# Optimization experiments

Hardware: AMD Instinct MI355X
Metric: run time of the kernel (lower is better)

## Reference

```python
import jax, jax.numpy as jnp
import numpy as np

NUM_PATCHES = 10
SIGMA = 4.0            # size_exp_deadzone
PAD_X = 16             # padding_deadzone_size_x
PAD_Y = 16             # padding_deadzone_size_y
DEADZONE_EXP = True
HARD_CUTOUT = True     # deadzone_hard_cutout == 1
HARD_CUTOUT_SIZE = 4.0


def setup_inputs() -> dict:
    key = jax.random.key(0)
    k1, k2, k3, k4 = jax.random.split(key, 4)
    B, C, H, W = 8, 1, 256, 256
    D, KH, KW = 64, 1, 33
    inp = {
        "input": jax.random.normal(k1, (B, C, H, W), dtype=jnp.float32),
        "dictionary_filter": jax.random.normal(k2, (64, C, 33, 33), dtype=jnp.float32),
        "dictionary": jax.random.normal(k3, (64, C, 33, 33), dtype=jnp.float32),
        "dictionary_prior": jax.random.uniform(k4, (64,), dtype=jnp.float32),
    }
    return inp


def _fourier_convolution(contour, dictionary_filter):
    # contour: [B,C,H,W], dictionary_filter: [D,C,kh,kw] (kh,kw odd)
    B, C, H, W = contour.shape
    D, _, kh, kw = dictionary_filter.shape
    filt = jnp.flip(dictionary_filter, axis=(-2, -1))
    padded = jnp.zeros((D, C, H, W), dtype=contour.dtype).at[:, :, :kh, :kw].set(filt)
    padded = jnp.roll(padded, shift=(-(kh // 2), -(kw // 2)), axis=(-2, -1))
    filt_fft = jnp.fft.rfft2(padded)                 # [D,C,H,W//2+1]
    contour_fft = jnp.fft.rfft2(contour)             # [B,C,H,W//2+1]
    # [B,D,C,H,W] -> sum over channel C -> [B,D,H,W]
    conv = jnp.fft.irfft2(contour_fft[:, None] * filt_fft[None], s=(H, W)).sum(axis=2)
    return conv


def reference(input, dictionary_filter, dictionary, dictionary_prior):
    B, C, H, W = input.shape
    dt = input.dtype
    conv = _fourier_convolution(input, dictionary_filter)  # [B,D,H,W]

    use_map = jnp.ones((B, H, W), dtype=dt)
    if PAD_X > 0:
        use_map = use_map.at[:, :PAD_X, :].set(0.0).at[:, -PAD_X:, :].set(0.0)
    if PAD_Y > 0:
        use_map = use_map.at[:, :, :PAD_Y].set(0.0).at[:, :, -PAD_Y:].set(0.0)

    xs = jnp.arange(H, dtype=dt)
    ys = jnp.arange(W, dtype=dt)
    batch_idx = jnp.arange(B)

    def step(use_map, _):
        # search tensor: conv * use_map * prior  -> [B,D,H,W]
        search = conv * use_map[:, None] * dictionary_prior[None, :, None, None]
        flat = search.reshape(B, -1)
        idx = jnp.argmax(flat, axis=1)                    # [B]
        ov0 = jnp.max(flat, axis=1)                       # saliency incl. prior
        d = idx // (H * W)
        rem = idx % (H * W)
        px = rem // W
        py = rem % W
        ov1 = conv[batch_idx, d, px, py]                  # raw overlap
        # deadzone centered at (px,py)
        dx = xs[None, :] - px[:, None].astype(dt)         # [B,H]
        dy = ys[None, :] - py[:, None].astype(dt)         # [B,W]
        dist2 = dx[:, :, None] ** 2 + dy[:, None, :] ** 2  # [B,H,W]
        if DEADZONE_EXP:
            tmap = 1.0 - jnp.exp(-dist2 / (2.0 * SIGMA ** 2))
        else:
            tmap = jnp.ones_like(dist2)
        if HARD_CUTOUT:
            tmap = tmap * jnp.where(dist2 <= HARD_CUTOUT_SIZE ** 2, 0.0, 1.0)
        new_use = use_map * tmap
        new_use = new_use / jnp.max(new_use, axis=(1, 2), keepdims=True)
        pos = jnp.stack([d, px, py], axis=1)              # [B,3]
        ov = jnp.stack([ov0, ov1], axis=1)                # [B,2]
        return new_use, (pos, ov)

    _, (pos, ov) = jax.lax.scan(step, use_map, None, length=NUM_PATCHES)
    position_found = jnp.transpose(pos, (1, 0, 2))  # [B, num_patches, 3] int
    overlap_found = jnp.transpose(ov, (1, 0, 2))    # [B, num_patches, 2]
    return position_found, overlap_found
```

## Files before the change

### kernel.cpp

```cpp
#include <hip/hip_runtime.h>

typedef unsigned long long u64;
typedef unsigned int u32;
typedef unsigned short ushort_t;

using f32x16 = __attribute__((ext_vector_type(16))) float;
using f32x4  = __attribute__((ext_vector_type(4))) float;
using short8 = __attribute__((ext_vector_type(8))) short;

#define NB 8
#define NPIX 65536
#define CAP1 8192
#define BAND 44.0f
#define CERT 43.0f

__device__ __forceinline__ u32 fsort(float f){
  u32 u = __float_as_uint(f);
  return (u & 0x80000000u) ? ~u : (u | 0x80000000u);
}
__device__ __forceinline__ float funsort(u32 s){
  u32 u = (s & 0x80000000u) ? (s ^ 0x80000000u) : ~s;
  return __uint_as_float(u);
}
__device__ __forceinline__ u32 rneb(float f){
  u32 x = __float_as_uint(f);
  return (x + 0x7fffu + ((x >> 16) & 1u)) >> 16;
}
__device__ __forceinline__ float bf2f(u32 h){ return __uint_as_float(h << 16); }

__global__ __launch_bounds__(256) void transpose_kernel(
    const float* __restrict__ filt, float* __restrict__ filtT,
    u32* __restrict__ ncand, u32* __restrict__ mmax)
{
  __shared__ float T[64][65];
  const int b = blockIdx.x;
  const int e0 = b * 64;
  const int ecnt = min(64, 1089 - e0);
  const int w = threadIdx.x >> 6, l = threadIdx.x & 63;
  if (b == 0 && threadIdx.x < 8){ ncand[threadIdx.x] = 0u; mmax[threadIdx.x] = 0u; }
  for (int d = w; d < 64; d += 4)
    if (l < ecnt) T[d][l] = filt[d * 1089 + e0 + l];
  __syncthreads();
  for (int r = w; r < ecnt; r += 4)
    filtT[(e0 + r) * 64 + l] = T[l][r];
}

__global__ __launch_bounds__(256) void prep_kernel(
    const float* __restrict__ filt, const float* __restrict__ filtT,
    const float* __restrict__ prior,
    ushort_t* __restrict__ afh, ushort_t* __restrict__ acolh,
    float* __restrict__ fcorner, float* __restrict__ priorR,
    float* __restrict__ filtT4, float* __restrict__ filtC)
{
  int t = blockIdx.x * 256 + threadIdx.x;
  for (int i = t; i < 67584; i += 16384){
    int j = i & 7; int fidx = i >> 3; int lane = fidx & 63; int rest = fidx >> 6;
    int dt = rest & 1; int kc = (rest >> 1) & 1; int fy = rest >> 2;
    int d = dt * 32 + (lane & 31);
    int fx = 16 * kc + 8 * (lane >> 5) + j;
    afh[i] = (ushort_t)rneb(filt[d * 1089 + fy * 33 + fx]);
  }
  for (int i = t; i < 2048; i += 16384){
    int j = i & 7; int fidx = i >> 3; int lane = fidx & 63; int rest = fidx >> 6;
    int dt = rest & 1; int kc = rest >> 1;
    int d = dt * 32 + (lane & 31);
    int fy = 16 * kc + 8 * (lane >> 5) + j;
    acolh[i] = (ushort_t)rneb(filt[d * 1089 + fy * 33 + 32]);
  }
  for (int i = t; i < 2048; i += 16384){
    int reg = i & 15; int rest = i >> 4; int lane = rest & 63; int dt = rest >> 6;
    int d = dt * 32 + (reg & 3) + 8 * (reg >> 2) + 4 * (lane >> 5);
    fcorner[i] = filt[d * 1089 + 1088];
    priorR[i] = prior[d];
  }
  for (int i = t; i < 67584; i += 16384){
    int e = i & 3; int d = (i >> 2) & 63; int q = (i >> 8) & 7; int fy = i >> 11;
    filtT4[i] = filtT[(fy * 33 + 4 * q + e) * 64 + d];
  }
  for (int i = t; i < 2112; i += 16384){
    int d = i & 63; int fy = i >> 6;
    filtC[i] = filtT[(fy * 33 + 32) * 64 + d];
  }
}

__device__ __forceinline__ u32 funnel(u32 hi, u32 lo, int sh){
  return (u32)((((u64)hi << 32) | (u64)lo) >> sh);
}
template<int J>
__device__ __forceinline__ short8 extractf(uint4 P0, uint4 P1, int sh){
  u32 W[8] = {P0.x, P0.y, P0.z, P0.w, P1.x, P1.y, P1.z, P1.w};
  uint4 t;
  t.x = funnel(W[J + 1], W[J + 0], sh);
  t.y = funnel(W[J + 2], W[J + 1], sh);
  t.z = funnel(W[J + 3], W[J + 2], sh);
  t.w = funnel(W[J + 4], W[J + 3], sh);
  return __builtin_bit_cast(short8, t);
}
__device__ __forceinline__ f32x16 zero16(){
  f32x16 v;
  #pragma unroll
  for (int i = 0; i < 16; ++i) v[i] = 0.f;
  return v;
}

template<int J>
__device__ __forceinline__ void conv_body(
    const char* ldsc, const ushort_t* lds16, int w, int l, int tX,
    const short8* __restrict__ afh8, const short8* __restrict__ acol8,
    const f32x4* __restrict__ fcp, const f32x4* __restrict__ prp,
    u64* __restrict__ pb, int sh)
{
  const int c = l & 31, h = l >> 5;
  const int y0 = w;
  int cob0[2], cob1[2];
  #pragma unroll
  for (int kc = 0; kc < 2; ++kc){
    int yp = (y0 + 8 * c + 16 * kc + 8 * h - 16) & 255;
    int b0 = yp >> 3, b1 = (b0 + 1) & 31;
    cob0[kc] = b0 * 16; cob1[kc] = b1 * 16;
  }
  const int cc = (y0 + 8 * c + 16) & 255;

#define LA(DST, FY)                                                           \
  { _Pragma("unroll")                                                         \
    for (int kc = 0; kc < 2; ++kc)                                            \
      _Pragma("unroll")                                                       \
      for (int dt = 0; dt < 2; ++dt)                                          \
        DST[kc][dt] = afh8[(((FY) * 2 + kc) * 2 + dt) * 64 + l]; }

#define LW(S, ROWI)                                                           \
  { const char* rb_ = ldsc + (ROWI) * 512;                                    \
    s##S##k0p0 = *(const uint4*)(rb_ + cob0[0]);                              \
    s##S##k0p1 = *(const uint4*)(rb_ + cob1[0]);                              \
    s##S##k1p0 = *(const uint4*)(rb_ + cob0[1]);                              \
    s##S##k1p1 = *(const uint4*)(rb_ + cob1[1]); }

#define CPH(SA, SB, ACUR, ANXT, FYP, DOPF)                                    \
  { if (DOPF){ LA(ANXT, FYP) }                                                \
    short8 b0k0 = extractf<J>(s##SA##k0p0, s##SA##k0p1, sh);                  \
    short8 b0k1 = extractf<J>(s##SA##k1p0, s##SA##k1p1, sh);                  \
    short8 b1k0 = extractf<J>(s##SB##k0p0, s##SB##k0p1, sh);                  \
    short8 b1k1 = extractf<J>(s##SB##k1p0, s##SB##k1p1, sh);                  \
    acc[0][0] = __builtin_amdgcn_mfma_f32_32x32x16_bf16(ACUR[0][0], b0k0, acc[0][0], 0, 0, 0); \
    acc[0][0] = __builtin_amdgcn_mfma_f32_32x32x16_bf16(ACUR[1][0], b0k1, acc[0][0], 0, 0, 0); \
    acc[0][1] = __builtin_amdgcn_mfma_f32_32x32x16_bf16(ACUR[0][1], b0k0, acc[0][1], 0, 0, 0); \
    acc[0][1] = __builtin_amdgcn_mfma_f32_32x32x16_bf16(ACUR[1][1], b0k1, acc[0][1], 0, 0, 0); \
    acc[1][0] = __builtin_amdgcn_mfma_f32_32x32x16_bf16(ACUR[0][0], b1k0, acc[1][0], 0, 0, 0); \
    acc[1][0] = __builtin_amdgcn_mfma_f32_32x32x16_bf16(ACUR[1][0], b1k1, acc[1][0], 0, 0, 0); \
    acc[1][1] = __builtin_amdgcn_mfma_f32_32x32x16_bf16(ACUR[0][1], b1k0, acc[1][1], 0, 0, 0); \
    acc[1][1] = __builtin_amdgcn_mfma_f32_32x32x16_bf16(ACUR[1][1], b1k1, acc[1][1], 0, 0, 0); }

  for (int g0 = 0; g0 < 2; ++g0){
    const int r0 = g0 * 2;
    f32x16 acc[2][2];
    #pragma unroll
    for (int nr = 0; nr < 2; ++nr)
      #pragma unroll
      for (int dt = 0; dt < 2; ++dt) acc[nr][dt] = zero16();

    uint4 s0k0p0, s0k0p1, s0k1p0, s0k1p1;
    uint4 s1k0p0, s1k0p1, s1k1p0, s1k1p1;
    short8 aA[2][2], aB[2][2];

    LW(0, r0)
    LW(1, r0 + 1)
    LA(aA, 0)

    #pragma unroll 1
    for (int fy2 = 0; fy2 < 32; fy2 += 2){
      CPH(0, 1, aA, aB, fy2 + 1, true)
      LW(0, r0 + fy2 + 2)
      CPH(1, 0, aB, aA, fy2 + 2, true)
      LW(1, r0 + fy2 + 3)
    }
    CPH(0, 1, aA, aB, 0, false)

    #pragma unroll
    for (int nr = 0; nr < 2; ++nr){
      #pragma unroll
      for (int kc = 0; kc < 2; ++kc){
        int base = (r0 + nr + 16 * kc + 8 * h) * 512 + cc * 2;
        u32 v0 = *(const ushort_t*)(ldsc + base + 0 * 512);
        u32 v1 = *(const ushort_t*)(ldsc + base + 1 * 512);
        u32 v2 = *(const ushort_t*)(ldsc + base + 2 * 512);
        u32 v3 = *(const ushort_t*)(ldsc + base + 3 * 512);
        u32 v4 = *(const ushort_t*)(ldsc + base + 4 * 512);
        u32 v5 = *(const ushort_t*)(ldsc + base + 5 * 512);
        u32 v6 = *(const ushort_t*)(ldsc + base + 6 * 512);
        u32 v7 = *(const ushort_t*)(ldsc + base + 7 * 512);
        uint4 t;
        t.x = v0 | (v1 << 16); t.y = v2 | (v3 << 16);
        t.z = v4 | (v5 << 16); t.w = v6 | (v7 << 16);
        short8 Bc = __builtin_bit_cast(short8, t);
        #pragma unroll
        for (int dt = 0; dt < 2; ++dt)
          acc[nr][dt] = __builtin_amdgcn_mfma_f32_32x32x16_bf16(
              acol8[(kc * 2 + dt) * 64 + l], Bc, acc[nr][dt], 0, 0, 0);
      }
    }

    #pragma unroll
    for (int nr = 0; nr < 2; ++nr){
      float cv = bf2f((u32)lds16[(r0 + nr + 32) * 256 + cc]);
      float bv = -3e38f; int bd = 0;
      #pragma unroll
      for (int dt = 0; dt < 2; ++dt){
        #pragma unroll
        for (int q = 0; q < 4; ++q){
          f32x4 fc4 = fcp[(dt * 64 + l) * 4 + q];
          f32x4 pr4 = prp[(dt * 64 + l) * 4 + q];
          #pragma unroll
          for (int e = 0; e < 4; ++e){
            int reg = q * 4 + e;
            float s = (acc[nr][dt][reg] + fc4[e] * cv) * pr4[e];
            int d = dt * 32 + e + 8 * q + 4 * h;
            if (s > bv || (s == bv && d < bd)){ bv = s; bd = d; }
          }
        }
      }
      int x = tX + r0 + nr;
      int y = y0 + 8 * c;
      u64 key = ((u64)fsort(bv) << 32) | (u64)(63 - bd);
      u64 other = __shfl_xor(key, 32);
      if (other > key) key = other;
      if (h == 0) pb[(x << 8) | y] = key;
    }
  }
#undef CPH
#undef LW
#undef LA
}

__global__ __launch_bounds__(512) void conv_mfma(
    const float* __restrict__ input,
    const ushort_t* __restrict__ afh, const ushort_t* __restrict__ acolh,
    const float* __restrict__ fcorner, const float* __restrict__ priorR,
    u64* __restrict__ packed)
{
  __shared__ ushort_t lds[9216];
  const int bS = blockIdx.x;
  const int b  = blockIdx.y;
  const int tX = bS * 4;
  const int tid = threadIdx.x;

  const float* inb = input + b * NPIX;
  for (int k = tid; k < 1152; k += 512){
    int r = k >> 5, u = k & 31;
    int gx = (tX - 16 + r) & 255;
    const float* src = inb + (gx << 8) + (u << 3);
    float4 v1 = *(const float4*)(src);
    float4 v2 = *(const float4*)(src + 4);
    uint4 t;
    t.x = rneb(v1.x) | (rneb(v1.y) << 16);
    t.y = rneb(v1.z) | (rneb(v1.w) << 16);
    t.z = rneb(v2.x) | (rneb(v2.y) << 16);
    t.w = rneb(v2.z) | (rneb(v2.w) << 16);
    *(uint4*)((char*)lds + r * 512 + u * 16) = t;
  }
  __syncthreads();

  const int w = tid >> 6, l = tid & 63;
  u64* pb = packed + b * NPIX;
  const int sh = 16 * (w & 1);
  const char* ldsc = (const char*)lds;
  const short8* afh8 = (const short8*)afh;
  const short8* acol8 = (const short8*)acolh;
  const f32x4* fcp = (const f32x4*)fcorner;
  const f32x4* prp = (const f32x4*)priorR;

  switch ((w >> 1) & 3){
    case 0: conv_body<0>(ldsc, lds, w, l, tX, afh8, acol8, fcp, prp, pb, sh); break;
    case 1: conv_body<1>(ldsc, lds, w, l, tX, afh8, acol8, fcp, prp, pb, sh); break;
    case 2: conv_body<2>(ldsc, lds, w, l, tX, afh8, acol8, fcp, prp, pb, sh); break;
    default: conv_body<3>(ldsc, lds, w, l, tX, afh8, acol8, fcp, prp, pb, sh); break;
  }
}

__global__ __launch_bounds__(256) void bmax_kernel(const u64* __restrict__ packed,
                                                   u32* __restrict__ mmax){
  const int b = blockIdx.y, blk = blockIdx.x, tid = threadIdx.x;
  const u32* ph = (const u32*)(packed + b * NPIX);
  u32 m = 0;
  for (int k = tid; k < 2048; k += 256) m = max(m, ph[2 * (blk * 2048 + k) + 1]);
  __shared__ u32 red[256];
  red[tid] = m; __syncthreads();
  for (int s = 128; s > 0; s >>= 1){
    if (tid < s) red[tid] = max(red[tid], red[tid + s]);
    __syncthreads();
  }
  if (tid == 0) atomicMax(&mmax[b], red[0]);
}

__global__ __launch_bounds__(256) void collect_kernel(const u64* __restrict__ packed,
    const u32* __restrict__ mmax, u32* __restrict__ ncand, u32* __restrict__ cand){
  const int b = blockIdx.y, blk = blockIdx.x, tid = threadIdx.x;
  u32 tu = fsort(funsort(mmax[b]) - BAND);
  const u32* ph = (const u32*)(packed + b * NPIX);
  for (int k = tid; k < 2048; k += 256){
    int p = blk * 2048 + k;
    int px = p >> 8, py = p & 255;
    u32 v = ph[2 * p + 1];
    if (v >= tu && px >= 16 && px < 240 && py >= 16 && py < 240){
      u32 slot = atomicAdd(&ncand[b], 1u);
      if (slot < CAP1) cand[b * CAP1 + slot] = (u32)p;
    }
  }
}

__global__ __launch_bounds__(256) void rerank_kernel(
    const float* __restrict__ input, const float* __restrict__ filtT4,
    const float* __restrict__ filtC, const float* __restrict__ prior,
    const u32* __restrict__ ncand, const u32* __restrict__ cand,
    u64* __restrict__ packed)
{
  const int lane = threadIdx.x & 63;
  const int b = blockIdx.y;
  const int ws = blockIdx.x * 4 + (threadIdx.x >> 6);
  int n = (int)min(ncand[b], (u32)CAP1);
  float pv = prior[lane];
  for (int i = ws; i < n; i += 512){
    int p = (int)cand[b * CAP1 + i];
    int px = p >> 8;
    int yc = (p & 255) - 16;
    float s0 = 0.f, s1 = 0.f, s2 = 0.f, s3 = 0.f;
    for (int fy = 0; fy < 33; ++fy){
      const float* ir = input + b * NPIX + ((px + fy - 16) << 8) + yc;
      const float* ft = filtT4 + fy * 2048 + lane * 4;
      #pragma unroll
      for (int q = 0; q < 8; ++q){
        const float4 fv = *(const float4*)(ft + q * 256);
        s0 = fmaf(fv.x, ir[4*q+0], s0);
        s1 = fmaf(fv.y, ir[4*q+1], s1);
        s2 = fmaf(fv.z, ir[4*q+2], s2);
        s3 = fmaf(fv.w, ir[4*q+3], s3);
      }
      s0 = fmaf(filtC[fy * 64 + lane], ir[32], s0);
    }
    float s = (s0 + s2) + (s1 + s3);
    u64 key = ((u64)fsort(s * pv) << 32) | (u64)(63 - lane);
    #pragma unroll
    for (int off = 32; off; off >>= 1){
      u64 o = __shfl_down(key, off);
      if (o > key) key = o;
    }
    if (lane == 0) packed[b * NPIX + p] = key;
  }
}

__global__ __launch_bounds__(1024) void greedy_sl(
    const u64* __restrict__ packed, const float* __restrict__ prior,
    const u32* __restrict__ ncand, const u32* __restrict__ cand,
    const u32* __restrict__ mmax, float* __restrict__ out)
{
  const int b = blockIdx.x;
  const int tid = threadIdx.x;
  const u64* pb = packed + b * NPIX;
  const int n = (int)min(ncand[b], (u32)CAP1);

  int cp[8]; float cv[8];
  #pragma unroll
  for (int k = 0; k < 8; ++k){
    int idx = tid + k * 1024;
    if (idx < n){ cp[k] = (int)cand[b * CAP1 + idx]; cv[k] = funsort((u32)(pb[cp[k]] >> 32)); }
    else        { cp[k] = 0; cv[k] = -3e38f; }
  }

  __shared__ u64 warr[16];
  __shared__ int spx, spy, okf;
  __shared__ float v10s;
  if (tid == 0){ spx = -100000; spy = -100000; }
  __syncthreads();

  for (int t = 0; t < 10; ++t){
    const int px = spx, py = spy;
    if (px >= 0){
      #pragma unroll
      for (int k = 0; k < 8; ++k){
        if (tid + k * 1024 < n){
          float dx = (float)((cp[k] >> 8) - px), dy = (float)((cp[k] & 255) - py);
          float d2 = dx * dx + dy * dy;
          float tmap = 1.f - __expf(d2 * -0.03125f);
          if (d2 <= 16.f) tmap = 0.f;
          cv[k] *= tmap;
        }
      }
    }
    u64 key = 0ull;
    #pragma unroll
    for (int k = 0; k < 8; ++k){
      u64 kk = ((u64)fsort(cv[k]) << 32) | (u64)(0xFFFFu ^ (u32)cp[k]);
      if (kk > key) key = kk;
    }
    #pragma unroll
    for (int off = 32; off; off >>= 1){
      u64 o = __shfl_down(key, off);
      if (o > key) key = o;
    }
    if ((tid & 63) == 0) warr[tid >> 6] = key;
    __syncthreads();
    if (tid < 64){
      u64 k2 = (tid < 16) ? warr[tid] : 0ull;
      #pragma unroll
      for (int off = 8; off; off >>= 1){
        u64 o = __shfl_down(k2, off);
        if (o > k2) k2 = o;
      }
      if (tid == 0){
        int id = 0xFFFF ^ (int)(k2 & 0xFFFFull);
        float v = funsort((u32)(k2 >> 32));
        u64 pk = pb[id];
        int d = 63 - (int)(pk & 63ull);
        float bvv = funsort((u32)(pk >> 32));
        int xx = id >> 8, yy = id & 255;
        out[b * 30 + t * 3 + 0] = (float)d;
        out[b * 30 + t * 3 + 1] = (float)xx;
        out[b * 30 + t * 3 + 2] = (float)yy;
        out[240 + b * 20 + t * 2 + 0] = v;
        out[240 + b * 20 + t * 2 + 1] = bvv / prior[d];
        spx = xx; spy = yy;
        if (t == 9) v10s = v;
      }
    }
    __syncthreads();
  }

  if (tid == 0)
    okf = (ncand[b] <= (u32)CAP1 && v10s >= funsort(mmax[b]) - CERT) ? 1 : 0;
  __syncthreads();
  if (okf) return;

  {
    const int x = tid >> 2;
    const int ybase = (tid & 3) << 6;
    const int pbase = (x << 8) + ybase;
    float s[64];
    const bool rowin = (x >= 16 && x < 240);
    #pragma unroll
    for (int i2 = 0; i2 < 32; ++i2){
      uint4 two = *(const uint4*)(pb + pbase + 2 * i2);
      int y = ybase + 2 * i2;
      s[2*i2+0] = (rowin && y+0 >= 16 && y+0 < 240) ? funsort(two.y) : 0.0f;
      s[2*i2+1] = (rowin && y+1 >= 16 && y+1 < 240) ? funsort(two.w) : 0.0f;
    }
    float tm = -3e38f; int tp = pbase;
    #pragma unroll
    for (int i = 0; i < 64; ++i){
      if (s[i] > tm){ tm = s[i]; tp = pbase + i; }
    }
    if (tid == 0){ spx = -100000; spy = -100000; }
    __syncthreads();
    for (int t = 0; t < 10; ++t){
      const int px = spx, py = spy;
      if (px >= 0){
        int dxr = x - px;
        if (dxr >= -24 && dxr <= 24){
          int lo = py - 24 - ybase;
          int hi = py + 24 - ybase;
          if (lo < 64 && hi >= 0){
            float dx2 = (float)(dxr * dxr);
            tm = -3e38f; tp = pbase;
            #pragma unroll
            for (int i = 0; i < 64; ++i){
              if (i >= lo && i <= hi){
                float dy = (float)(ybase + i - py);
                float d2 = dx2 + dy * dy;
                float tmap = 1.f - __expf(d2 * -0.03125f);
                if (d2 <= 16.f) tmap = 0.f;
                s[i] *= tmap;
              }
              if (s[i] > tm){ tm = s[i]; tp = pbase + i; }
            }
          }
        }
      }
      u64 key = ((u64)fsort(tm) << 32) | (u64)(0xFFFFu ^ (u32)tp);
      #pragma unroll
      for (int off = 32; off; off >>= 1){
        u64 o = __shfl_down(key, off);
        if (o > key) key = o;
      }
      if ((tid & 63) == 0) warr[tid >> 6] = key;
      __syncthreads();
      if (tid < 64){
        u64 k2 = (tid < 16) ? warr[tid] : 0ull;
        #pragma unroll
        for (int off = 8; off; off >>= 1){
          u64 o = __shfl_down(k2, off);
          if (o > k2) k2 = o;
        }
        if (tid == 0){
          int id = 0xFFFF ^ (int)(k2 & 0xFFFFull);
          float v = funsort((u32)(k2 >> 32));
          u64 pk = pb[id];
          int d = 63 - (int)(pk & 63ull);
          float bvv = funsort((u32)(pk >> 32));
          int xx = id >> 8, yy = id & 255;
          out[b * 30 + t * 3 + 0] = (float)d;
          out[b * 30 + t * 3 + 1] = (float)xx;
          out[b * 30 + t * 3 + 2] = (float)yy;
          out[240 + b * 20 + t * 2 + 0] = v;
          out[240 + b * 20 + t * 2 + 1] = bvv / prior[d];
          spx = xx; spy = yy;
        }
      }
      __syncthreads();
    }
  }
}

extern "C" void kernel_launch(void* const* d_in, const int* in_sizes, int n_in,
                              void* d_out, int out_size, void* d_ws, size_t ws_size,
                              hipStream_t stream)
{
  const float* input = (const float*)d_in[0];
  const float* filt  = (const float*)d_in[1];
  const float* prior = (const float*)d_in[3];
  float* out = (float*)d_out;

  char* ws = (char*)d_ws;
  u64*      packed  = (u64*)(ws);
  u32*      ncand   = (u32*)  (ws + 4194304);
  u32*      mmax    = (u32*)  (ws + 4194368);
  ushort_t* afh     = (ushort_t*)(ws + 4194432);
  ushort_t* acolh   = (ushort_t*)(ws + 4329600);
  float*    fcorner = (float*)(ws + 4333696);
  float*    priorR  = (float*)(ws + 4341888);
  u32*      cand    = (u32*)  (ws + 4350080);
  float*    filtT4  = (float*)(ws + 4612224);
  float*    filtC   = (float*)(ws + 4882560);
  float*    filtT   = (float*)(ws + 4891008);

  transpose_kernel<<<18, 256, 0, stream>>>(filt, filtT, ncand, mmax);
  prep_kernel<<<64, 256, 0, stream>>>(filt, filtT, prior, afh, acolh,
                                      fcorner, priorR, filtT4, filtC);
  conv_mfma<<<dim3(64, NB), 512, 0, stream>>>(input, afh, acolh, fcorner, priorR, packed);
  bmax_kernel<<<dim3(32, NB), 256, 0, stream>>>(packed, mmax);
  collect_kernel<<<dim3(32, NB), 256, 0, stream>>>(packed, mmax, ncand, cand);
  rerank_kernel<<<dim3(128, NB), 256, 0, stream>>>(input, filtT4, filtC, prior,
                                                   ncand, cand, packed);
  greedy_sl<<<NB, 1024, 0, stream>>>(packed, prior, ncand, cand, mmax, out);
}
```

Before: 250.9 us.

## Derive candidate threshold from tenth-best disjoint block max instead of global max band

Replaces the global-max reduction plus fixed band with a lower bound taken from 16 disjoint 16x16 sub-blocks. The tenth-largest block max minus a small epsilon becomes the candidate threshold, which should admit far fewer candidates into the bf16 rerank and greedy stages. It also drops the post-greedy certification check and the full-image fallback whenever candidates fit in the capacity. The tighter threshold rests on assumptions about the bf16 approximation error and deadzone suppression, so correctness could be at risk if the error exceeds the epsilon.

```diff
diff --git a/kernel.cpp b/kernel.cpp
--- a/kernel.cpp
+++ b/kernel.cpp
@@ -11,8 +11,7 @@
 #define NB 8
 #define NPIX 65536
 #define CAP1 8192
-#define BAND 44.0f
-#define CERT 43.0f
+#define EPS2 8.0f
 
 __device__ __forceinline__ u32 fsort(float f){
   u32 u = __float_as_uint(f);
@@ -30,14 +29,14 @@
 
 __global__ __launch_bounds__(256) void transpose_kernel(
     const float* __restrict__ filt, float* __restrict__ filtT,
-    u32* __restrict__ ncand, u32* __restrict__ mmax)
+    u32* __restrict__ ncand)
 {
   __shared__ float T[64][65];
   const int b = blockIdx.x;
   const int e0 = b * 64;
   const int ecnt = min(64, 1089 - e0);
   const int w = threadIdx.x >> 6, l = threadIdx.x & 63;
-  if (b == 0 && threadIdx.x < 8){ ncand[threadIdx.x] = 0u; mmax[threadIdx.x] = 0u; }
+  if (b == 0 && threadIdx.x < 8) ncand[threadIdx.x] = 0u;
   for (int d = w; d < 64; d += 4)
     if (l < ecnt) T[d][l] = filt[d * 1089 + e0 + l];
   __syncthreads();
@@ -276,25 +275,45 @@
   }
 }
 
-__global__ __launch_bounds__(256) void bmax_kernel(const u64* __restrict__ packed,
-                                                   u32* __restrict__ mmax){
+__global__ __launch_bounds__(256) void lbound_kernel(
+    const u64* __restrict__ packed, float* __restrict__ thr)
+{
+  const int b = blockIdx.x;
+  const int tid = threadIdx.x;
+  const u32* ph = (const u32*)(packed + b * NPIX);
+  __shared__ u32 red[256];
+  __shared__ u32 q16[16];
+  const int r = tid >> 4, cY = tid & 15;
+  for (int sc = 0; sc < 16; ++sc){
+    int x = 24 + ((sc >> 2) << 6) + r;
+    int y = 24 + ((sc & 3) << 6) + cY;
+    red[tid] = ph[2 * ((x << 8) | y) + 1];
+    __syncthreads();
+    for (int s = 128; s > 0; s >>= 1){
+      if (tid < s) red[tid] = max(red[tid], red[tid + s]);
+      __syncthreads();
+    }
+    if (tid == 0) q16[sc] = red[0];
+    __syncthreads();
+  }
+  if (tid == 0){
+    u32 q[16];
+    for (int i = 0; i < 16; ++i) q[i] = q16[i];
+    u32 tenth = 0;
+    for (int k = 0; k < 10; ++k){
+      int bi = 0;
+      for (int i = 1; i < 16; ++i) if (q[i] > q[bi]) bi = i;
+      tenth = q[bi];
+      q[bi] = 0;
+    }
+    thr[b] = funsort(tenth) - EPS2;
+  }
+}
+
+__global__ __launch_bounds__(256) void collect_kernel(const u64* __restrict__ packed,
+    const float* __restrict__ thr, u32* __restrict__ ncand, u32* __restrict__ cand){
   const int b = blockIdx.y, blk = blockIdx.x, tid = threadIdx.x;
-  const u32* ph = (const u32*)(packed + b * NPIX);
-  u32 m = 0;
-  for (int k = tid; k < 2048; k += 256) m = max(m, ph[2 * (blk * 2048 + k) + 1]);
-  __shared__ u32 red[256];
-  red[tid] = m; __syncthreads();
-  for (int s = 128; s > 0; s >>= 1){
-    if (tid < s) red[tid] = max(red[tid], red[tid + s]);
-    __syncthreads();
-  }
-  if (tid == 0) atomicMax(&mmax[b], red[0]);
-}
-
-__global__ __launch_bounds__(256) void collect_kernel(const u64* __restrict__ packed,
-    const u32* __restrict__ mmax, u32* __restrict__ ncand, u32* __restrict__ cand){
-  const int b = blockIdx.y, blk = blockIdx.x, tid = threadIdx.x;
-  u32 tu = fsort(funsort(mmax[b]) - BAND);
+  u32 tu = fsort(thr[b]);
   const u32* ph = (const u32*)(packed + b * NPIX);
   for (int k = tid; k < 2048; k += 256){
     int p = blk * 2048 + k;
@@ -350,7 +369,7 @@
 __global__ __launch_bounds__(1024) void greedy_sl(
     const u64* __restrict__ packed, const float* __restrict__ prior,
     const u32* __restrict__ ncand, const u32* __restrict__ cand,
-    const u32* __restrict__ mmax, float* __restrict__ out)
+    float* __restrict__ out)
 {
   const int b = blockIdx.x;
   const int tid = threadIdx.x;
@@ -367,67 +386,62 @@
 
   __shared__ u64 warr[16];
   __shared__ int spx, spy, okf;
-  __shared__ float v10s;
-  if (tid == 0){ spx = -100000; spy = -100000; }
+  if (tid == 0){ spx = -100000; spy = -100000; okf = (ncand[b] <= (u32)CAP1); }
   __syncthreads();
-
-  for (int t = 0; t < 10; ++t){
-    const int px = spx, py = spy;
-    if (px >= 0){
+  if (okf){
+    for (int t = 0; t < 10; ++t){
+      const int px = spx, py = spy;
+      if (px >= 0){
+        #pragma unroll
+        for (int k = 0; k < 8; ++k){
+          if (tid + k * 1024 < n){
+            float dx = (float)((cp[k] >> 8) - px), dy = (float)((cp[k] & 255) - py);
+            float d2 = dx * dx + dy * dy;
+            float tmap = 1.f - __expf(d2 * -0.03125f);
+            if (d2 <= 16.f) tmap = 0.f;
+            cv[k] *= tmap;
+          }
+        }
+      }
+      u64 key = 0ull;
       #pragma unroll
       for (int k = 0; k < 8; ++k){
-        if (tid + k * 1024 < n){
-          float dx = (float)((cp[k] >> 8) - px), dy = (float)((cp[k] & 255) - py);
-          float d2 = dx * dx + dy * dy;
-          float tmap = 1.f - __expf(d2 * -0.03125f);
-          if (d2 <= 16.f) tmap = 0.f;
-          cv[k] *= tmap;
-        }
-      }
-    }
-    u64 key = 0ull;
-    #pragma unroll
-    for (int k = 0; k < 8; ++k){
-      u64 kk = ((u64)fsort(cv[k]) << 32) | (u64)(0xFFFFu ^ (u32)cp[k]);
-      if (kk > key) key = kk;
-    }
-    #pragma unroll
-    for (int off = 32; off; off >>= 1){
-      u64 o = __shfl_down(key, off);
-      if (o > key) key = o;
-    }
-    if ((tid & 63) == 0) warr[tid >> 6] = key;
-    __syncthreads();
-    if (tid < 64){
-      u64 k2 = (tid < 16) ? warr[tid] : 0ull;
-      #pragma unroll
-      for (int off = 8; off; off >>= 1){
-        u64 o = __shfl_down(k2, off);
-        if (o > k2) k2 = o;
-      }
-      if (tid == 0){
-        int id = 0xFFFF ^ (int)(k2 & 0xFFFFull);
-        float v = funsort((u32)(k2 >> 32));
-        u64 pk = pb[id];
-        int d = 63 - (int)(pk & 63ull);
-        float bvv = funsort((u32)(pk >> 32));
-        int xx = id >> 8, yy = id & 255;
-        out[b * 30 + t * 3 + 0] = (float)d;
-        out[b * 30 + t * 3 + 1] = (float)xx;
-        out[b * 30 + t * 3 + 2] = (float)yy;
-        out[240 + b * 20 + t * 2 + 0] = v;
-        out[240 + b * 20 + t * 2 + 1] = bvv / prior[d];
-        spx = xx; spy = yy;
-        if (t == 9) v10s = v;
-      }
-    }
-    __syncthreads();
-  }
-
-  if (tid == 0)
-    okf = (ncand[b] <= (u32)CAP1 && v10s >= funsort(mmax[b]) - CERT) ? 1 : 0;
-  __syncthreads();
-  if (okf) return;
+        u64 kk = ((u64)fsort(cv[k]) << 32) | (u64)(0xFFFFu ^ (u32)cp[k]);
+        if (kk > key) key = kk;
+      }
+      #pragma unroll
+      for (int off = 32; off; off >>= 1){
+        u64 o = __shfl_down(key, off);
+        if (o > key) key = o;
+      }
+      if ((tid & 63) == 0) warr[tid >> 6] = key;
+      __syncthreads();
+      if (tid < 64){
+        u64 k2 = (tid < 16) ? warr[tid] : 0ull;
+        #pragma unroll
+        for (int off = 8; off; off >>= 1){
+          u64 o = __shfl_down(k2, off);
+          if (o > k2) k2 = o;
+        }
+        if (tid == 0){
+          int id = 0xFFFF ^ (int)(k2 & 0xFFFFull);
+          float v = funsort((u32)(k2 >> 32));
+          u64 pk = pb[id];
+          int d = 63 - (int)(pk & 63ull);
+          float bvv = funsort((u32)(pk >> 32));
+          int xx = id >> 8, yy = id & 255;
+          out[b * 30 + t * 3 + 0] = (float)d;
+          out[b * 30 + t * 3 + 1] = (float)xx;
+          out[b * 30 + t * 3 + 2] = (float)yy;
+          out[240 + b * 20 + t * 2 + 0] = v;
+          out[240 + b * 20 + t * 2 + 1] = bvv / prior[d];
+          spx = xx; spy = yy;
+        }
+      }
+      __syncthreads();
+    }
+    return;
+  }
 
   {
     const int x = tid >> 2;
@@ -447,7 +461,6 @@
     for (int i = 0; i < 64; ++i){
       if (s[i] > tm){ tm = s[i]; tp = pbase + i; }
     }
-    if (tid == 0){ spx = -100000; spy = -100000; }
     __syncthreads();
     for (int t = 0; t < 10; ++t){
       const int px = spx, py = spy;
@@ -520,7 +533,7 @@
   char* ws = (char*)d_ws;
   u64*      packed  = (u64*)(ws);
   u32*      ncand   = (u32*)  (ws + 4194304);
-  u32*      mmax    = (u32*)  (ws + 4194368);
+  float*    thr     = (float*)(ws + 4194368);
   ushort_t* afh     = (ushort_t*)(ws + 4194432);
   ushort_t* acolh   = (ushort_t*)(ws + 4329600);
   float*    fcorner = (float*)(ws + 4333696);
@@ -530,13 +543,13 @@
   float*    filtC   = (float*)(ws + 4882560);
   float*    filtT   = (float*)(ws + 4891008);
 
-  transpose_kernel<<<18, 256, 0, stream>>>(filt, filtT, ncand, mmax);
+  transpose_kernel<<<18, 256, 0, stream>>>(filt, filtT, ncand);
   prep_kernel<<<64, 256, 0, stream>>>(filt, filtT, prior, afh, acolh,
                                       fcorner, priorR, filtT4, filtC);
   conv_mfma<<<dim3(64, NB), 512, 0, stream>>>(input, afh, acolh, fcorner, priorR, packed);
-  bmax_kernel<<<dim3(32, NB), 256, 0, stream>>>(packed, mmax);
-  collect_kernel<<<dim3(32, NB), 256, 0, stream>>>(packed, mmax, ncand, cand);
+  lbound_kernel<<<NB, 256, 0, stream>>>(packed, thr);
+  collect_kernel<<<dim3(32, NB), 256, 0, stream>>>(packed, thr, ncand, cand);
   rerank_kernel<<<dim3(128, NB), 256, 0, stream>>>(input, filtT4, filtC, prior,
                                                    ncand, cand, packed);
-  greedy_sl<<<NB, 1024, 0, stream>>>(packed, prior, ncand, cand, mmax, out);
-}
+  greedy_sl<<<NB, 1024, 0, stream>>>(packed, prior, ncand, cand, out);
+}
```

Measured after the change: 239.9 us. 4.4% less time.

## Add pre-greedy pass to tighten rerank candidate threshold

Applied to the files above, without the earlier changes.

Adds a greedy pass over the approximate (bf16 MFMA) scores to estimate the 10th selected value, then collects a second, smaller candidate set within a slack of that value. Only those candidates get the exact fp32 rerank, and the final greedy runs over at most 4096 candidates instead of 8192. This trades two extra small kernel launches and a duplicated greedy for less rerank work, and it relies on tighter certification margins that can force the full-image fallback more often.

```diff
diff --git a/kernel.cpp b/kernel.cpp
--- a/kernel.cpp
+++ b/kernel.cpp
@@ -11,8 +11,10 @@
 #define NB 8
 #define NPIX 65536
 #define CAP1 8192
-#define BAND 44.0f
-#define CERT 43.0f
+#define CAP2 4096
+#define T1    24.0f
+#define SLACK 12.0f
+#define CERTF 10.0f
 
 __device__ __forceinline__ u32 fsort(float f){
   u32 u = __float_as_uint(f);
@@ -30,14 +32,15 @@
 
 __global__ __launch_bounds__(256) void transpose_kernel(
     const float* __restrict__ filt, float* __restrict__ filtT,
-    u32* __restrict__ ncand, u32* __restrict__ mmax)
+    u32* __restrict__ nc16, u32* __restrict__ mmax)
 {
   __shared__ float T[64][65];
   const int b = blockIdx.x;
   const int e0 = b * 64;
   const int ecnt = min(64, 1089 - e0);
   const int w = threadIdx.x >> 6, l = threadIdx.x & 63;
-  if (b == 0 && threadIdx.x < 8){ ncand[threadIdx.x] = 0u; mmax[threadIdx.x] = 0u; }
+  if (b == 0 && threadIdx.x < 16) nc16[threadIdx.x] = 0u;
+  if (b == 0 && threadIdx.x < 8)  mmax[threadIdx.x] = 0u;
   for (int d = w; d < 64; d += 4)
     if (l < ecnt) T[d][l] = filt[d * 1089 + e0 + l];
   __syncthreads();
@@ -291,71 +294,31 @@
   if (tid == 0) atomicMax(&mmax[b], red[0]);
 }
 
-__global__ __launch_bounds__(256) void collect_kernel(const u64* __restrict__ packed,
-    const u32* __restrict__ mmax, u32* __restrict__ ncand, u32* __restrict__ cand){
+__global__ __launch_bounds__(256) void collect1_kernel(const u64* __restrict__ packed,
+    const u32* __restrict__ mmax, u32* __restrict__ nc16, u32* __restrict__ cand){
   const int b = blockIdx.y, blk = blockIdx.x, tid = threadIdx.x;
-  u32 tu = fsort(funsort(mmax[b]) - BAND);
+  u32 tu = fsort(funsort(mmax[b]) - T1);
   const u32* ph = (const u32*)(packed + b * NPIX);
   for (int k = tid; k < 2048; k += 256){
     int p = blk * 2048 + k;
     int px = p >> 8, py = p & 255;
     u32 v = ph[2 * p + 1];
     if (v >= tu && px >= 16 && px < 240 && py >= 16 && py < 240){
-      u32 slot = atomicAdd(&ncand[b], 1u);
+      u32 slot = atomicAdd(&nc16[b], 1u);
       if (slot < CAP1) cand[b * CAP1 + slot] = (u32)p;
     }
   }
 }
 
-__global__ __launch_bounds__(256) void rerank_kernel(
-    const float* __restrict__ input, const float* __restrict__ filtT4,
-    const float* __restrict__ filtC, const float* __restrict__ prior,
-    const u32* __restrict__ ncand, const u32* __restrict__ cand,
-    u64* __restrict__ packed)
-{
-  const int lane = threadIdx.x & 63;
-  const int b = blockIdx.y;
-  const int ws = blockIdx.x * 4 + (threadIdx.x >> 6);
-  int n = (int)min(ncand[b], (u32)CAP1);
-  float pv = prior[lane];
-  for (int i = ws; i < n; i += 512){
-    int p = (int)cand[b * CAP1 + i];
-    int px = p >> 8;
-    int yc = (p & 255) - 16;
-    float s0 = 0.f, s1 = 0.f, s2 = 0.f, s3 = 0.f;
-    for (int fy = 0; fy < 33; ++fy){
-      const float* ir = input + b * NPIX + ((px + fy - 16) << 8) + yc;
-      const float* ft = filtT4 + fy * 2048 + lane * 4;
-      #pragma unroll
-      for (int q = 0; q < 8; ++q){
-        const float4 fv = *(const float4*)(ft + q * 256);
-        s0 = fmaf(fv.x, ir[4*q+0], s0);
-        s1 = fmaf(fv.y, ir[4*q+1], s1);
-        s2 = fmaf(fv.z, ir[4*q+2], s2);
-        s3 = fmaf(fv.w, ir[4*q+3], s3);
-      }
-      s0 = fmaf(filtC[fy * 64 + lane], ir[32], s0);
-    }
-    float s = (s0 + s2) + (s1 + s3);
-    u64 key = ((u64)fsort(s * pv) << 32) | (u64)(63 - lane);
-    #pragma unroll
-    for (int off = 32; off; off >>= 1){
-      u64 o = __shfl_down(key, off);
-      if (o > key) key = o;
-    }
-    if (lane == 0) packed[b * NPIX + p] = key;
-  }
-}
-
-__global__ __launch_bounds__(1024) void greedy_sl(
-    const u64* __restrict__ packed, const float* __restrict__ prior,
-    const u32* __restrict__ ncand, const u32* __restrict__ cand,
-    const u32* __restrict__ mmax, float* __restrict__ out)
+__global__ __launch_bounds__(1024) void pregreedy_kernel(
+    const u64* __restrict__ packed, const u32* __restrict__ nc16,
+    const u32* __restrict__ cand, const u32* __restrict__ mmax,
+    float* __restrict__ tmin)
 {
   const int b = blockIdx.x;
   const int tid = threadIdx.x;
   const u64* pb = packed + b * NPIX;
-  const int n = (int)min(ncand[b], (u32)CAP1);
+  const int n = (int)min(nc16[b], (u32)CAP1);
 
   int cp[8]; float cv[8];
   #pragma unroll
@@ -407,27 +370,17 @@
       }
       if (tid == 0){
         int id = 0xFFFF ^ (int)(k2 & 0xFFFFull);
-        float v = funsort((u32)(k2 >> 32));
-        u64 pk = pb[id];
-        int d = 63 - (int)(pk & 63ull);
-        float bvv = funsort((u32)(pk >> 32));
-        int xx = id >> 8, yy = id & 255;
-        out[b * 30 + t * 3 + 0] = (float)d;
-        out[b * 30 + t * 3 + 1] = (float)xx;
-        out[b * 30 + t * 3 + 2] = (float)yy;
-        out[240 + b * 20 + t * 2 + 0] = v;
-        out[240 + b * 20 + t * 2 + 1] = bvv / prior[d];
-        spx = xx; spy = yy;
-        if (t == 9) v10s = v;
+        spx = id >> 8; spy = id & 255;
+        if (t == 9) v10s = funsort((u32)(k2 >> 32));
       }
     }
     __syncthreads();
   }
 
   if (tid == 0)
-    okf = (ncand[b] <= (u32)CAP1 && v10s >= funsort(mmax[b]) - CERT) ? 1 : 0;
+    okf = (nc16[b] <= (u32)CAP1 && v10s >= funsort(mmax[b]) - (T1 - 1.0f)) ? 1 : 0;
   __syncthreads();
-  if (okf) return;
+  if (okf){ if (tid == 0) tmin[b] = v10s; return; }
 
   {
     const int x = tid >> 2;
@@ -490,6 +443,214 @@
         }
         if (tid == 0){
           int id = 0xFFFF ^ (int)(k2 & 0xFFFFull);
+          spx = id >> 8; spy = id & 255;
+          if (t == 9) tmin[b] = funsort((u32)(k2 >> 32));
+        }
+      }
+      __syncthreads();
+    }
+  }
+}
+
+__global__ __launch_bounds__(256) void collect2_kernel(const u64* __restrict__ packed,
+    const float* __restrict__ tmin, u32* __restrict__ nc16, u32* __restrict__ cand2){
+  const int b = blockIdx.y, blk = blockIdx.x, tid = threadIdx.x;
+  u32 tu = fsort(tmin[b] - SLACK);
+  const u32* ph = (const u32*)(packed + b * NPIX);
+  for (int k = tid; k < 2048; k += 256){
+    int p = blk * 2048 + k;
+    int px = p >> 8, py = p & 255;
+    u32 v = ph[2 * p + 1];
+    if (v >= tu && px >= 16 && px < 240 && py >= 16 && py < 240){
+      u32 slot = atomicAdd(&nc16[8 + b], 1u);
+      if (slot < CAP2) cand2[b * CAP2 + slot] = (u32)p;
+    }
+  }
+}
+
+__global__ __launch_bounds__(256) void rerank_kernel(
+    const float* __restrict__ input, const float* __restrict__ filtT4,
+    const float* __restrict__ filtC, const float* __restrict__ prior,
+    const u32* __restrict__ nc16, const u32* __restrict__ cand2,
+    u64* __restrict__ packed)
+{
+  const int lane = threadIdx.x & 63;
+  const int b = blockIdx.y;
+  const int ws = blockIdx.x * 4 + (threadIdx.x >> 6);
+  int n = (int)min(nc16[8 + b], (u32)CAP2);
+  float pv = prior[lane];
+  for (int i = ws; i < n; i += 512){
+    int p = (int)cand2[b * CAP2 + i];
+    int px = p >> 8;
+    int yc = (p & 255) - 16;
+    float s0 = 0.f, s1 = 0.f, s2 = 0.f, s3 = 0.f;
+    for (int fy = 0; fy < 33; ++fy){
+      const float* ir = input + b * NPIX + ((px + fy - 16) << 8) + yc;
+      const float* ft = filtT4 + fy * 2048 + lane * 4;
+      #pragma unroll
+      for (int q = 0; q < 8; ++q){
+        const float4 fv = *(const float4*)(ft + q * 256);
+        s0 = fmaf(fv.x, ir[4*q+0], s0);
+        s1 = fmaf(fv.y, ir[4*q+1], s1);
+        s2 = fmaf(fv.z, ir[4*q+2], s2);
+        s3 = fmaf(fv.w, ir[4*q+3], s3);
+      }
+      s0 = fmaf(filtC[fy * 64 + lane], ir[32], s0);
+    }
+    float s = (s0 + s2) + (s1 + s3);
+    u64 key = ((u64)fsort(s * pv) << 32) | (u64)(63 - lane);
+    #pragma unroll
+    for (int off = 32; off; off >>= 1){
+      u64 o = __shfl_down(key, off);
+      if (o > key) key = o;
+    }
+    if (lane == 0) packed[b * NPIX + p] = key;
+  }
+}
+
+__global__ __launch_bounds__(1024) void greedy_sl(
+    const u64* __restrict__ packed, const float* __restrict__ prior,
+    const u32* __restrict__ nc16, const u32* __restrict__ cand2,
+    const float* __restrict__ tmin, float* __restrict__ out)
+{
+  const int b = blockIdx.x;
+  const int tid = threadIdx.x;
+  const u64* pb = packed + b * NPIX;
+  const int n = (int)min(nc16[8 + b], (u32)CAP2);
+
+  int cp[4]; float cv[4];
+  #pragma unroll
+  for (int k = 0; k < 4; ++k){
+    int idx = tid + k * 1024;
+    if (idx < n){ cp[k] = (int)cand2[b * CAP2 + idx]; cv[k] = funsort((u32)(pb[cp[k]] >> 32)); }
+    else        { cp[k] = 0; cv[k] = -3e38f; }
+  }
+
+  __shared__ u64 warr[16];
+  __shared__ int spx, spy, okf;
+  __shared__ float v10s;
+  if (tid == 0){ spx = -100000; spy = -100000; }
+  __syncthreads();
+
+  for (int t = 0; t < 10; ++t){
+    const int px = spx, py = spy;
+    if (px >= 0){
+      #pragma unroll
+      for (int k = 0; k < 4; ++k){
+        if (tid + k * 1024 < n){
+          float dx = (float)((cp[k] >> 8) - px), dy = (float)((cp[k] & 255) - py);
+          float d2 = dx * dx + dy * dy;
+          float tmap = 1.f - __expf(d2 * -0.03125f);
+          if (d2 <= 16.f) tmap = 0.f;
+          cv[k] *= tmap;
+        }
+      }
+    }
+    u64 key = 0ull;
+    #pragma unroll
+    for (int k = 0; k < 4; ++k){
+      u64 kk = ((u64)fsort(cv[k]) << 32) | (u64)(0xFFFFu ^ (u32)cp[k]);
+      if (kk > key) key = kk;
+    }
+    #pragma unroll
+    for (int off = 32; off; off >>= 1){
+      u64 o = __shfl_down(key, off);
+      if (o > key) key = o;
+    }
+    if ((tid & 63) == 0) warr[tid >> 6] = key;
+    __syncthreads();
+    if (tid < 64){
+      u64 k2 = (tid < 16) ? warr[tid] : 0ull;
+      #pragma unroll
+      for (int off = 8; off; off >>= 1){
+        u64 o = __shfl_down(k2, off);
+        if (o > k2) k2 = o;
+      }
+      if (tid == 0){
+        int id = 0xFFFF ^ (int)(k2 & 0xFFFFull);
+        float v = funsort((u32)(k2 >> 32));
+        u64 pk = pb[id];
+        int d = 63 - (int)(pk & 63ull);
+        float bvv = funsort((u32)(pk >> 32));
+        int xx = id >> 8, yy = id & 255;
+        out[b * 30 + t * 3 + 0] = (float)d;
+        out[b * 30 + t * 3 + 1] = (float)xx;
+        out[b * 30 + t * 3 + 2] = (float)yy;
+        out[240 + b * 20 + t * 2 + 0] = v;
+        out[240 + b * 20 + t * 2 + 1] = bvv / prior[d];
+        spx = xx; spy = yy;
+        if (t == 9) v10s = v;
+      }
+    }
+    __syncthreads();
+  }
+
+  if (tid == 0)
+    okf = (nc16[8 + b] <= (u32)CAP2 && v10s >= tmin[b] - CERTF) ? 1 : 0;
+  __syncthreads();
+  if (okf) return;
+
+  {
+    const int x = tid >> 2;
+    const int ybase = (tid & 3) << 6;
+    const int pbase = (x << 8) + ybase;
+    float s[64];
+    const bool rowin = (x >= 16 && x < 240);
+    #pragma unroll
+    for (int i2 = 0; i2 < 32; ++i2){
+      uint4 two = *(const uint4*)(pb + pbase + 2 * i2);
+      int y = ybase + 2 * i2;
+      s[2*i2+0] = (rowin && y+0 >= 16 && y+0 < 240) ? funsort(two.y) : 0.0f;
+      s[2*i2+1] = (rowin && y+1 >= 16 && y+1 < 240) ? funsort(two.w) : 0.0f;
+    }
+    float tm = -3e38f; int tp = pbase;
+    #pragma unroll
+    for (int i = 0; i < 64; ++i){
+      if (s[i] > tm){ tm = s[i]; tp = pbase + i; }
+    }
+    if (tid == 0){ spx = -100000; spy = -100000; }
+    __syncthreads();
+    for (int t = 0; t < 10; ++t){
+      const int px = spx, py = spy;
+      if (px >= 0){
+        int dxr = x - px;
+        if (dxr >= -24 && dxr <= 24){
+          int lo = py - 24 - ybase;
+          int hi = py + 24 - ybase;
+          if (lo < 64 && hi >= 0){
+            float dx2 = (float)(dxr * dxr);
+            tm = -3e38f; tp = pbase;
+            #pragma unroll
+            for (int i = 0; i < 64; ++i){
+              if (i >= lo && i <= hi){
+                float dy = (float)(ybase + i - py);
+                float d2 = dx2 + dy * dy;
+                float tmap = 1.f - __expf(d2 * -0.03125f);
+                if (d2 <= 16.f) tmap = 0.f;
+                s[i] *= tmap;
+              }
+              if (s[i] > tm){ tm = s[i]; tp = pbase + i; }
+            }
+          }
+        }
+      }
+      u64 key = ((u64)fsort(tm) << 32) | (u64)(0xFFFFu ^ (u32)tp);
+      #pragma unroll
+      for (int off = 32; off; off >>= 1){
+        u64 o = __shfl_down(key, off);
+        if (o > key) key = o;
+      }
+      if ((tid & 63) == 0) warr[tid >> 6] = key;
+      __syncthreads();
+      if (tid < 64){
+        u64 k2 = (tid < 16) ? warr[tid] : 0ull;
+        #pragma unroll
+        for (int off = 8; off; off >>= 1){
+          u64 o = __shfl_down(k2, off);
+          if (o > k2) k2 = o;
+        }
+        if (tid == 0){
+          int id = 0xFFFF ^ (int)(k2 & 0xFFFFull);
           float v = funsort((u32)(k2 >> 32));
           u64 pk = pb[id];
           int d = 63 - (int)(pk & 63ull);
@@ -519,8 +680,9 @@
 
   char* ws = (char*)d_ws;
   u64*      packed  = (u64*)(ws);
-  u32*      ncand   = (u32*)  (ws + 4194304);
+  u32*      nc16    = (u32*)  (ws + 4194304);
   u32*      mmax    = (u32*)  (ws + 4194368);
+  float*    tmin    = (float*)(ws + 4194400);
   ushort_t* afh     = (ushort_t*)(ws + 4194432);
   ushort_t* acolh   = (ushort_t*)(ws + 4329600);
   float*    fcorner = (float*)(ws + 4333696);
@@ -529,14 +691,17 @@
   float*    filtT4  = (float*)(ws + 4612224);
   float*    filtC   = (float*)(ws + 4882560);
   float*    filtT   = (float*)(ws + 4891008);
-
-  transpose_kernel<<<18, 256, 0, stream>>>(filt, filtT, ncand, mmax);
+  u32*      cand2   = (u32*)  (ws + 5169792);
+
+  transpose_kernel<<<18, 256, 0, stream>>>(filt, filtT, nc16, mmax);
   prep_kernel<<<64, 256, 0, stream>>>(filt, filtT, prior, afh, acolh,
                                       fcorner, priorR, filtT4, filtC);
   conv_mfma<<<dim3(64, NB), 512, 0, stream>>>(input, afh, acolh, fcorner, priorR, packed);
   bmax_kernel<<<dim3(32, NB), 256, 0, stream>>>(packed, mmax);
-  collect_kernel<<<dim3(32, NB), 256, 0, stream>>>(packed, mmax, ncand, cand);
+  collect1_kernel<<<dim3(32, NB), 256, 0, stream>>>(packed, mmax, nc16, cand);
+  pregreedy_kernel<<<NB, 1024, 0, stream>>>(packed, nc16, cand, mmax, tmin);
+  collect2_kernel<<<dim3(32, NB), 256, 0, stream>>>(packed, tmin, nc16, cand2);
   rerank_kernel<<<dim3(128, NB), 256, 0, stream>>>(input, filtT4, filtC, prior,
-                                                   ncand, cand, packed);
-  greedy_sl<<<NB, 1024, 0, stream>>>(packed, prior, ncand, cand, mmax, out);
-}
+                                                   nc16, cand2, packed);
+  greedy_sl<<<NB, 1024, 0, stream>>>(packed, prior, nc16, cand2, tmin, out);
+}
```

New measurement: 264.3 us. 5.3% more time.
